# Kernel tuning notes

Hardware: AMD Instinct MI355X
Metric: run time of the kernel (lower is better)

The kernel has to match this reference:

```python
import jax, jax.numpy as jnp
import numpy as np
import math

B, S, D, H = 2, 2048, 4096, 32
HD = D // H          # 128 head dim
HALF = HD // 2       # 64 rotary pairs
AL = 10              # adapter length


def setup_inputs() -> dict:
    key = jax.random.key(0)
    ks = jax.random.split(key, 8)
    sc = 0.02
    x = jax.random.normal(ks[0], (B, S, D), jnp.float32)
    adapter = jax.random.normal(ks[1], (B, AL, D), jnp.float32)
    wq = jax.random.normal(ks[2], (D, D), jnp.float32) * sc
    wk = jax.random.normal(ks[3], (D, D), jnp.float32) * sc
    wv = jax.random.normal(ks[4], (D, D), jnp.float32) * sc
    wo = jax.random.normal(ks[5], (D, D), jnp.float32) * sc
    gate = jax.random.normal(ks[6], (1, H, 1, 1), jnp.float32) * 0.1
    # rotary frequencies (LLaMA convention), freqs_cis = exp(i * t * f)
    inv_freq = 1.0 / (10000.0 ** (np.arange(0, HD, 2).astype(np.float32) / HD))
    ang = np.outer(np.arange(S, dtype=np.float32), inv_freq)  # [S, HALF]
    cos = jnp.asarray(np.cos(ang), jnp.float32)
    sin = jnp.asarray(np.sin(ang), jnp.float32)
    # additive causal mask [1,1,S,S]
    mask = jnp.triu(jnp.full((S, S), -1e9, jnp.float32), 1)[None, None]
    return {"x": x, "mask": mask, "cos": cos, "sin": sin, "wq": wq,
            "wk": wk, "wv": wv, "wo": wo, "gate": gate,
            "adapter": adapter, "start_pos": 0}


def _rope(t, cos, sin):
    # t: [B,S,H,HD]; complex rotate consecutive pairs
    tr = t.reshape(*t.shape[:-1], HALF, 2)
    t0, t1 = tr[..., 0], tr[..., 1]
    c = cos[None, :, None, :]  # [1,S,1,HALF]
    s = sin[None, :, None, :]
    r0 = t0 * c - t1 * s
    r1 = t0 * s + t1 * c
    return jnp.stack([r0, r1], axis=-1).reshape(t.shape)


def reference(x, mask, cos, sin, wq, wk, wv, wo, gate, adapter, start_pos):
    bsz, seqlen, _ = x.shape
    scale = 1.0 / math.sqrt(HD)
    xq = (x @ wq.T).reshape(bsz, seqlen, H, HD)
    xk = (x @ wk.T).reshape(bsz, seqlen, H, HD)
    xv = (x @ wv.T).reshape(bsz, seqlen, H, HD)
    xq = _rope(xq, cos, sin)
    xk = _rope(xk, cos, sin)
    # training path: keys/values = current tokens (start_pos == 0)
    q = xq.transpose(0, 2, 1, 3)   # [B,H,S,HD]
    k = xk.transpose(0, 2, 1, 3)
    v = xv.transpose(0, 2, 1, 3)
    scores = jnp.einsum('bhqd,bhkd->bhqk', q, k) * scale + mask
    scores = jax.nn.softmax(scores.astype(jnp.float32), axis=-1).astype(x.dtype)
    out = jnp.einsum('bhqk,bhkd->bhqd', scores, v)
    # gated adapter cross-attention (adapter_len > 1 branch)
    a_len = adapter.shape[1]
    a_v = (adapter @ wv.T).reshape(bsz, a_len, H, HD).transpose(0, 2, 1, 3)
    a_k = (adapter @ wk.T).reshape(bsz, a_len, H, HD).transpose(0, 2, 1, 3)
    a_scores = jnp.einsum('bhqd,bhkd->bhqk', q, a_k) * scale
    a_scores = jnp.tanh(gate) * jax.nn.softmax(
        a_scores.astype(jnp.float32), axis=-1).astype(x.dtype)
    out = out + jnp.einsum('bhqk,bhkd->bhqd', a_scores, a_v)
    out = out.transpose(0, 2, 1, 3).reshape(bsz, seqlen, -1)
    return out @ wo.T
```

## Files before the change

### kernel.cpp

```cpp
#include <hip/hip_runtime.h>
#include <hip/hip_bf16.h>
#include <stdint.h>

#define B_ 2
#define S_ 2048
#define D_ 4096
#define H_ 32
#define HD_ 128
#define HALF_ 64
#define AL_ 10
#define MROWS (B_*S_)

typedef __hip_bfloat16 bf16;
typedef __attribute__((ext_vector_type(8))) __bf16 bf16x8;
typedef __attribute__((ext_vector_type(4))) float f32x4;
typedef __attribute__((ext_vector_type(4))) unsigned short us4;

__device__ __forceinline__ void gld_lds16(const void* g, void* l) {
    __builtin_amdgcn_global_load_lds((const __attribute__((address_space(1))) void*)g,
                                     (__attribute__((address_space(3))) void*)l, 16, 0, 0);
}

__global__ void detect_dtype(const unsigned short* __restrict__ x, int* __restrict__ flag) {
    __shared__ int cnt;
    if (threadIdx.x == 0) cnt = 0;
    __syncthreads();
    int bad = 0;
#pragma unroll
    for (int i = 0; i < 16; i++) {
        unsigned int u = x[threadIdx.x * 16 + i];
        float v = __uint_as_float(u << 16);
        if (!(fabsf(v) < 1000.f)) bad++;
    }
    atomicAdd(&cnt, bad);
    __syncthreads();
    if (threadIdx.x == 0) flag[0] = (cnt > 64) ? 1 : 0;
}

__global__ void convert_bf16(const void* __restrict__ in, bf16* __restrict__ out,
                             const int* __restrict__ flag, int n) {
    int i = (blockIdx.x * 256 + threadIdx.x) * 4;
    if (i >= n) return;
    if (flag[0]) {
        float4 f = *(const float4*)((const float*)in + i);
        out[i + 0] = __float2bfloat16(f.x);
        out[i + 1] = __float2bfloat16(f.y);
        out[i + 2] = __float2bfloat16(f.z);
        out[i + 3] = __float2bfloat16(f.w);
    } else {
        *(us4*)(out + i) = *(const us4*)((const unsigned short*)in + i);
    }
}

template<int MODE>
__global__ __launch_bounds__(256) void gemm_bt(
    const bf16* __restrict__ A, const bf16* __restrict__ W,
    const bf16* __restrict__ cosb, const bf16* __restrict__ sinb,
    void* __restrict__ outv, const int* __restrict__ flag, int K)
{
    __shared__ __align__(16) bf16 sA[128*64];
    __shared__ __align__(16) bf16 sB[128*64];
    const int tid  = threadIdx.x;
    const int wave = tid >> 6, lane = tid & 63;
    const int quad = lane >> 4, col = lane & 15;
    const int m0 = blockIdx.y * 128, n0 = blockIdx.x * 128;
    const int wm = (wave >> 1) * 64, wn = (wave & 1) * 64;

    bool f32o = false;
    if (MODE == 2) f32o = (flag[0] != 0);

    f32x4 acc[4][4];
#pragma unroll
    for (int i = 0; i < 4; i++)
#pragma unroll
        for (int j = 0; j < 4; j++) acc[i][j] = {0.f, 0.f, 0.f, 0.f};

    for (int k0 = 0; k0 < K; k0 += 64) {
        __syncthreads();
#pragma unroll
        for (int i = 0; i < 4; i++) {
            int c   = i * 256 + tid;
            int row = c >> 3;
            int cc  = (c & 7) ^ (row & 7);
            gld_lds16(A + (size_t)(m0 + row) * K + k0 + cc * 8,
                      sA + (size_t)(i * 256 + wave * 64) * 8);
            gld_lds16(W + (size_t)(n0 + row) * K + k0 + cc * 8,
                      sB + (size_t)(i * 256 + wave * 64) * 8);
        }
        __syncthreads();

#pragma unroll
        for (int kk = 0; kk < 64; kk += 32) {
            bf16x8 af[4], bfr[4];
#pragma unroll
            for (int mt = 0; mt < 4; mt++) {
                int r  = wm + mt * 16 + col;
                int ck = ((kk >> 3) + quad) ^ (r & 7);
                af[mt] = *(const bf16x8*)(sA + r * 64 + ck * 8);
            }
#pragma unroll
            for (int nt = 0; nt < 4; nt++) {
                int r  = wn + nt * 16 + col;
                int ck = ((kk >> 3) + quad) ^ (r & 7);
                bfr[nt] = *(const bf16x8*)(sB + r * 64 + ck * 8);
            }
#pragma unroll
            for (int mt = 0; mt < 4; mt++)
#pragma unroll
                for (int nt = 0; nt < 4; nt++)
                    acc[mt][nt] = __builtin_amdgcn_mfma_f32_16x16x32_bf16(
                        af[mt], bfr[nt], acc[mt][nt], 0, 0, 0);
        }
    }

#pragma unroll
    for (int mt = 0; mt < 4; mt++) {
#pragma unroll
        for (int nt = 0; nt < 4; nt++) {
            int n = n0 + wn + nt * 16 + col;
#pragma unroll
            for (int e = 0; e < 4; e++) {
                int m   = m0 + wm + mt * 16 + quad * 4 + e;
                float v = acc[mt][nt][e];
                if (MODE == 2) {
                    if (f32o) ((float*)outv)[(size_t)m * D_ + n] = v;
                    else      ((bf16*)outv)[(size_t)m * D_ + n] = __float2bfloat16(v);
                } else {
                    int b = m >> 11, s = m & (S_ - 1);
                    int h = n >> 7,  hd = n & (HD_ - 1);
                    bf16* out = (bf16*)outv;
                    if (MODE == 0) {
                        float other = __shfl_xor(v, 1);
                        float c  = __bfloat162float(cosb[s * HALF_ + (hd >> 1)]);
                        float sn = __bfloat162float(sinb[s * HALF_ + (hd >> 1)]);
                        float r  = (hd & 1) ? (v * c + other * sn)
                                            : (v * c - other * sn);
                        out[((size_t)(b * H_ + h) * S_ + s) * HD_ + hd] = __float2bfloat16(r);
                    } else {
                        out[((size_t)(b * H_ + h) * HD_ + hd) * S_ + s] = __float2bfloat16(v);
                    }
                }
            }
        }
    }
}

__global__ __launch_bounds__(512, 4) void attn_fwd(
    const bf16* __restrict__ q, const bf16* __restrict__ k,
    const bf16* __restrict__ vT, bf16* __restrict__ o)
{
    __shared__ __align__(16) bf16 smem[40960];
    bf16* sP = smem + 32768;

    const int tid  = threadIdx.x, wave = tid >> 6, lane = tid & 63;
    const int quad = lane >> 4, col = lane & 15;
    const int qt = (gridDim.x - 1) - blockIdx.x;
    const int bh = blockIdx.y;
    const int q0 = qt * 128;
    const int row0 = q0 + wave * 16;
    const int rmax = row0 + 15;
    const bf16* qb = q  + (size_t)bh * S_ * HD_;
    const bf16* kb = k  + (size_t)bh * S_ * HD_;
    const bf16* vb = vT + (size_t)bh * HD_ * S_;

    bf16x8 qf[4];
#pragma unroll
    for (int kkI = 0; kkI < 4; kkI++)
        qf[kkI] = *(const bf16x8*)(qb + (size_t)(row0 + col) * HD_ + (kkI * 4 + quad) * 8);

    float mst[4], lst[4];
#pragma unroll
    for (int e = 0; e < 4; e++) { mst[e] = -1e30f; lst[e] = 0.f; }
    f32x4 oacc[8];
#pragma unroll
    for (int i = 0; i < 8; i++) oacc[i] = {0.f, 0.f, 0.f, 0.f};

#pragma unroll
    for (int i = 0; i < 2; i++) {
        int c = i * 512 + tid;
        int rowK = c >> 4, ccK = (c & 15) ^ (rowK & 7);
        gld_lds16(kb + (size_t)rowK * HD_ + ccK * 8,
                  smem + (size_t)(i * 512 + wave * 64) * 8);
        int rowV = c >> 3, ccV = (c & 7) ^ (rowV & 7);
        gld_lds16(vb + (size_t)rowV * S_ + ccV * 8,
                  smem + 16384 + (size_t)(i * 512 + wave * 64) * 8);
    }

    const float scale = 0.08838834764831845f;
    const int ktEnd = 2 * qt + 2;
    int cur = 0;

    for (int kt = 0; kt < ktEnd; kt++) {
        const int k0 = kt * 64;
        bf16* sKc = smem + cur * 8192;
        bf16* sVc = smem + 16384 + cur * 8192;

        if (kt + 1 < ktEnd) {
            const int kn = k0 + 64;
            bf16* sKn = smem + (cur ^ 1) * 8192;
            bf16* sVn = smem + 16384 + (cur ^ 1) * 8192;
#pragma unroll
            for (int i = 0; i < 2; i++) {
                int c = i * 512 + tid;
                int rowK = c >> 4, ccK = (c & 15) ^ (rowK & 7);
                gld_lds16(kb + (size_t)(kn + rowK) * HD_ + ccK * 8,
                          sKn + (size_t)(i * 512 + wave * 64) * 8);
                int rowV = c >> 3, ccV = (c & 7) ^ (rowV & 7);
                gld_lds16(vb + (size_t)rowV * S_ + kn + ccV * 8,
                          sVn + (size_t)(i * 512 + wave * 64) * 8);
            }
            asm volatile("s_waitcnt vmcnt(4)" ::: "memory");
        } else {
            asm volatile("s_waitcnt vmcnt(0)" ::: "memory");
        }
        asm volatile("s_barrier" ::: "memory");

        if (k0 <= rmax) {
            f32x4 sc[4];
#pragma unroll
            for (int nt = 0; nt < 4; nt++) sc[nt] = {0.f, 0.f, 0.f, 0.f};
            __builtin_amdgcn_s_setprio(1);
#pragma unroll
            for (int kkI = 0; kkI < 4; kkI++) {
#pragma unroll
                for (int nt = 0; nt < 4; nt++) {
                    int rk  = nt * 16 + col;
                    int ckk = (kkI * 4 + quad) ^ (rk & 7);
                    bf16x8 bk = *(const bf16x8*)(sKc + rk * 128 + ckk * 8);
                    sc[nt] = __builtin_amdgcn_mfma_f32_16x16x32_bf16(qf[kkI], bk, sc[nt], 0, 0, 0);
                }
            }
            __builtin_amdgcn_s_setprio(0);

            const bool diag = (k0 + 63 > row0);
#pragma unroll
            for (int nt = 0; nt < 4; nt++)
#pragma unroll
                for (int e = 0; e < 4; e++) {
                    float v = sc[nt][e] * scale;
                    if (diag && (k0 + nt * 16 + col > row0 + quad * 4 + e))
                        v = -1e30f;
                    sc[nt][e] = v;
                }

            float alpha_[4];
#pragma unroll
            for (int e = 0; e < 4; e++) {
                float mx = fmaxf(fmaxf(sc[0][e], sc[1][e]),
                                 fmaxf(sc[2][e], sc[3][e]));
#pragma unroll
                for (int off = 1; off < 16; off <<= 1) mx = fmaxf(mx, __shfl_xor(mx, off));
                float mnew = fmaxf(mst[e], mx);
                float al   = __expf(mst[e] - mnew);
                float rs   = 0.f;
                int prow = wave * 16 + quad * 4 + e;
#pragma unroll
                for (int nt = 0; nt < 4; nt++) {
                    float p = __expf(sc[nt][e] - mnew);
                    rs += p;
                    int pcol = nt * 16 + col;
                    int pc   = (pcol >> 3) ^ (prow & 7);
                    sP[prow * 64 + pc * 8 + (pcol & 7)] = __float2bfloat16(p);
                }
#pragma unroll
                for (int off = 1; off < 16; off <<= 1) rs += __shfl_xor(rs, off);
                lst[e] = lst[e] * al + rs;
                mst[e] = mnew;
                alpha_[e] = al;
            }
#pragma unroll
            for (int nt = 0; nt < 8; nt++)
#pragma unroll
                for (int e = 0; e < 4; e++) oacc[nt][e] *= alpha_[e];

            __builtin_amdgcn_s_setprio(1);
#pragma unroll
            for (int kkI = 0; kkI < 2; kkI++) {
                int rp  = wave * 16 + col;
                int ckp = (kkI * 4 + quad) ^ (rp & 7);
                bf16x8 pf = *(const bf16x8*)(sP + rp * 64 + ckp * 8);
#pragma unroll
                for (int nt = 0; nt < 8; nt++) {
                    int rv  = nt * 16 + col;
                    int ckv = (kkI * 4 + quad) ^ (rv & 7);
                    bf16x8 vf = *(const bf16x8*)(sVc + rv * 64 + ckv * 8);
                    oacc[nt] = __builtin_amdgcn_mfma_f32_16x16x32_bf16(pf, vf, oacc[nt], 0, 0, 0);
                }
            }
            __builtin_amdgcn_s_setprio(0);
        }

        asm volatile("s_barrier" ::: "memory");
        cur ^= 1;
    }

    const int b = bh >> 5, h = bh & (H_ - 1);
#pragma unroll
    for (int e = 0; e < 4; e++) {
        int s = q0 + wave * 16 + quad * 4 + e;
        float inv = 1.f / lst[e];
#pragma unroll
        for (int nt = 0; nt < 8; nt++) {
            int hd = nt * 16 + col;
            o[((size_t)(b * S_ + s) * H_ + h) * HD_ + hd] =
                __float2bfloat16(oacc[nt][e] * inv);
        }
    }
}

__global__ __launch_bounds__(256) void adapter_kv(
    const bf16* __restrict__ adp, const bf16* __restrict__ wk,
    const bf16* __restrict__ wv, float* __restrict__ ak, float* __restrict__ av)
{
    const int tid = threadIdx.x, wave = tid >> 6, lane = tid & 63;
    const int gid = blockIdx.x * 4 + wave;
    const int n = gid & (D_ - 1), b = gid >> 12;
    const bf16* w    = blockIdx.y ? wv : wk;
    float*      outp = blockIdx.y ? av : ak;

    float acc[AL_];
#pragma unroll
    for (int j = 0; j < AL_; j++) acc[j] = 0.f;

    for (int t = 0; t < 8; t++) {
        int kb = t * 512 + lane * 8;
        bf16x8 w8 = *(const bf16x8*)(w + (size_t)n * D_ + kb);
        float wf[8];
#pragma unroll
        for (int i = 0; i < 8; i++) wf[i] = (float)w8[i];
#pragma unroll
        for (int j = 0; j < AL_; j++) {
            bf16x8 a8 = *(const bf16x8*)(adp + (size_t)(b * AL_ + j) * D_ + kb);
            float s = 0.f;
#pragma unroll
            for (int i = 0; i < 8; i++) s += (float)a8[i] * wf[i];
            acc[j] += s;
        }
    }
#pragma unroll
    for (int j = 0; j < AL_; j++) {
        float v = acc[j];
#pragma unroll
        for (int off = 1; off < 64; off <<= 1) v += __shfl_xor(v, off);
        if (lane == 0) outp[(size_t)(b * AL_ + j) * D_ + n] = v;
    }
}

__global__ __launch_bounds__(256) void adapter_add(
    const bf16* __restrict__ q, const float* __restrict__ ak,
    const float* __restrict__ av, const bf16* __restrict__ gate,
    bf16* __restrict__ o)
{
    const int tid = threadIdx.x, wave = tid >> 6, lane = tid & 63;
    const int g = blockIdx.x * 4 + wave;
    const int s = g & (S_ - 1);
    const int h = (g >> 11) & (H_ - 1);
    const int b = g >> 16;
    const int hd = lane * 2;

    const bf16* qp = q + ((size_t)(b * H_ + h) * S_ + s) * HD_ + hd;
    float q0f = __bfloat162float(qp[0]);
    float q1f = __bfloat162float(qp[1]);
    const float scale = 0.08838834764831845f;

    float sc[AL_];
#pragma unroll
    for (int j = 0; j < AL_; j++) {
        const float* akp = ak + (size_t)(b * AL_ + j) * D_ + h * HD_ + hd;
        float p = q0f * akp[0] + q1f * akp[1];
#pragma unroll
        for (int off = 1; off < 64; off <<= 1) p += __shfl_xor(p, off);
        sc[j] = p * scale;
    }
    float mx = sc[0];
#pragma unroll
    for (int j = 1; j < AL_; j++) mx = fmaxf(mx, sc[j]);
    float sum = 0.f;
#pragma unroll
    for (int j = 0; j < AL_; j++) { sc[j] = __expf(sc[j] - mx); sum += sc[j]; }
    float wgt = tanhf(__bfloat162float(gate[h])) / sum;

    float a0 = 0.f, a1 = 0.f;
#pragma unroll
    for (int j = 0; j < AL_; j++) {
        const float* avp = av + (size_t)(b * AL_ + j) * D_ + h * HD_ + hd;
        a0 += sc[j] * avp[0];
        a1 += sc[j] * avp[1];
    }
    bf16* op = o + ((size_t)(b * S_ + s) * H_ + h) * HD_ + hd;
    op[0] = __float2bfloat16(__bfloat162float(op[0]) + wgt * a0);
    op[1] = __float2bfloat16(__bfloat162float(op[1]) + wgt * a1);
}

extern "C" void kernel_launch(void* const* d_in, const int* in_sizes, int n_in,
                              void* d_out, int out_size, void* d_ws, size_t ws_size,
                              hipStream_t stream)
{
    const void* x_raw    = d_in[0];
    const void* cos_raw  = d_in[2];
    const void* sin_raw  = d_in[3];
    const void* wq_raw   = d_in[4];
    const void* wk_raw   = d_in[5];
    const void* wv_raw   = d_in[6];
    const void* wo_raw   = d_in[7];
    const void* gate_raw = d_in[8];
    const void* adp_raw  = d_in[9];

    const size_t NE = (size_t)B_ * S_ * D_;
    const int    CS = S_ * HALF_;
    const int    AD = B_ * AL_ * D_;

    bf16* xc   = (bf16*)d_ws;
    bf16* wqc  = xc  + NE;
    bf16* wkc  = wqc + NE;
    bf16* wvc  = wkc + NE;
    bf16* woc  = wvc + NE;
    bf16* qb   = woc + NE;
    bf16* kb   = qb  + NE;
    bf16* vb   = kb  + NE;
    bf16* cosc = vb  + NE;
    bf16* sinc = cosc + CS;
    bf16* adpc = sinc + CS;
    bf16* gatec= adpc + AD;
    float* akb = (float*)(gatec + 32);
    float* avb = akb + AD;
    int*  flag = (int*)(avb + AD);
    bf16* ab   = xc;

    dim3 blk(256);
    detect_dtype<<<1, 256, 0, stream>>>((const unsigned short*)x_raw, flag);

    convert_bf16<<<dim3((int)(NE/4 + 255) / 256), blk, 0, stream>>>(x_raw,  xc,  flag, (int)NE);
    convert_bf16<<<dim3((int)(NE/4 + 255) / 256), blk, 0, stream>>>(wq_raw, wqc, flag, (int)NE);
    convert_bf16<<<dim3((int)(NE/4 + 255) / 256), blk, 0, stream>>>(wk_raw, wkc, flag, (int)NE);
    convert_bf16<<<dim3((int)(NE/4 + 255) / 256), blk, 0, stream>>>(wv_raw, wvc, flag, (int)NE);
    convert_bf16<<<dim3((int)(NE/4 + 255) / 256), blk, 0, stream>>>(wo_raw, woc, flag, (int)NE);
    convert_bf16<<<dim3((CS/4 + 255) / 256), blk, 0, stream>>>(cos_raw,  cosc, flag, CS);
    convert_bf16<<<dim3((CS/4 + 255) / 256), blk, 0, stream>>>(sin_raw,  sinc, flag, CS);
    convert_bf16<<<dim3((AD/4 + 255) / 256), blk, 0, stream>>>(adp_raw,  adpc, flag, AD);
    convert_bf16<<<dim3(1), blk, 0, stream>>>(gate_raw, gatec, flag, 32);

    dim3 gg(D_ / 128, MROWS / 128);
    gemm_bt<0><<<gg, blk, 0, stream>>>(xc, wqc, cosc, sinc, qb, flag, D_);
    gemm_bt<0><<<gg, blk, 0, stream>>>(xc, wkc, cosc, sinc, kb, flag, D_);
    gemm_bt<1><<<gg, blk, 0, stream>>>(xc, wvc, cosc, sinc, vb, flag, D_);
    adapter_kv<<<dim3(2048, 2), blk, 0, stream>>>(adpc, wkc, wvc, akb, avb);
    attn_fwd<<<dim3(S_ / 128, B_ * H_), dim3(512), 0, stream>>>(qb, kb, vb, ab);
    adapter_add<<<dim3(B_ * H_ * S_ / 4), blk, 0, stream>>>(qb, akb, avb, gatec, ab);
    gemm_bt<2><<<gg, blk, 0, stream>>>(ab, woc, cosc, sinc, d_out, flag, D_);
}
```

Measured before the change: 1.435 ms.

## Fold softmax scale into Q, pair causal tiles per block, lazy rescale

The softmax scale is folded into the Q projection epilogue, so both attention kernels skip the per-score multiply. Each attention block now processes two query tiles (qt and NQT-1-qt), which balances the causal work across blocks and halves the grid. The online softmax uses exp2 with a log2e prefactor and skips the output rescale unless some row max grew by more than a threshold. The sP swizzle is also changed to reduce LDS bank conflicts. Rounding Q to bf16 after scaling slightly changes numerics, and the lazy rescale lets exponentials exceed 1 before normalisation.

```diff
diff --git a/kernel.cpp b/kernel.cpp
--- a/kernel.cpp
+++ b/kernel.cpp
@@ -10,6 +10,7 @@
 #define HALF_ 64
 #define AL_ 10
 #define MROWS (B_*S_)
+#define NQT_ (S_/128)
 
 typedef __hip_bfloat16 bf16;
 typedef __attribute__((ext_vector_type(8))) __bf16 bf16x8;
@@ -56,7 +57,7 @@
 __global__ __launch_bounds__(256) void gemm_bt(
     const bf16* __restrict__ A, const bf16* __restrict__ W,
     const bf16* __restrict__ cosb, const bf16* __restrict__ sinb,
-    void* __restrict__ outv, const int* __restrict__ flag, int K)
+    void* __restrict__ outv, const int* __restrict__ flag, int K, float oscale)
 {
     __shared__ __align__(16) bf16 sA[128*64];
     __shared__ __align__(16) bf16 sB[128*64];
@@ -135,7 +136,8 @@
                         float sn = __bfloat162float(sinb[s * HALF_ + (hd >> 1)]);
                         float r  = (hd & 1) ? (v * c + other * sn)
                                             : (v * c - other * sn);
-                        out[((size_t)(b * H_ + h) * S_ + s) * HD_ + hd] = __float2bfloat16(r);
+                        out[((size_t)(b * H_ + h) * S_ + s) * HD_ + hd] =
+                            __float2bfloat16(r * oscale);
                     } else {
                         out[((size_t)(b * H_ + h) * HD_ + hd) * S_ + s] = __float2bfloat16(v);
                     }
@@ -154,156 +156,177 @@
 
     const int tid  = threadIdx.x, wave = tid >> 6, lane = tid & 63;
     const int quad = lane >> 4, col = lane & 15;
-    const int qt = (gridDim.x - 1) - blockIdx.x;
     const int bh = blockIdx.y;
-    const int q0 = qt * 128;
-    const int row0 = q0 + wave * 16;
-    const int rmax = row0 + 15;
+    const int b = bh >> 5, h = bh & (H_ - 1);
     const bf16* qb = q  + (size_t)bh * S_ * HD_;
     const bf16* kb = k  + (size_t)bh * S_ * HD_;
     const bf16* vb = vT + (size_t)bh * HD_ * S_;
-
-    bf16x8 qf[4];
-#pragma unroll
-    for (int kkI = 0; kkI < 4; kkI++)
-        qf[kkI] = *(const bf16x8*)(qb + (size_t)(row0 + col) * HD_ + (kkI * 4 + quad) * 8);
-
-    float mst[4], lst[4];
-#pragma unroll
-    for (int e = 0; e < 4; e++) { mst[e] = -1e30f; lst[e] = 0.f; }
-    f32x4 oacc[8];
-#pragma unroll
-    for (int i = 0; i < 8; i++) oacc[i] = {0.f, 0.f, 0.f, 0.f};
-
-#pragma unroll
-    for (int i = 0; i < 2; i++) {
-        int c = i * 512 + tid;
-        int rowK = c >> 4, ccK = (c & 15) ^ (rowK & 7);
-        gld_lds16(kb + (size_t)rowK * HD_ + ccK * 8,
-                  smem + (size_t)(i * 512 + wave * 64) * 8);
-        int rowV = c >> 3, ccV = (c & 7) ^ (rowV & 7);
-        gld_lds16(vb + (size_t)rowV * S_ + ccV * 8,
-                  smem + 16384 + (size_t)(i * 512 + wave * 64) * 8);
-    }
-
-    const float scale = 0.08838834764831845f;
-    const int ktEnd = 2 * qt + 2;
-    int cur = 0;
-
-    for (int kt = 0; kt < ktEnd; kt++) {
-        const int k0 = kt * 64;
-        bf16* sKc = smem + cur * 8192;
-        bf16* sVc = smem + 16384 + cur * 8192;
-
-        if (kt + 1 < ktEnd) {
-            const int kn = k0 + 64;
-            bf16* sKn = smem + (cur ^ 1) * 8192;
-            bf16* sVn = smem + 16384 + (cur ^ 1) * 8192;
-#pragma unroll
-            for (int i = 0; i < 2; i++) {
-                int c = i * 512 + tid;
-                int rowK = c >> 4, ccK = (c & 15) ^ (rowK & 7);
-                gld_lds16(kb + (size_t)(kn + rowK) * HD_ + ccK * 8,
-                          sKn + (size_t)(i * 512 + wave * 64) * 8);
-                int rowV = c >> 3, ccV = (c & 7) ^ (rowV & 7);
-                gld_lds16(vb + (size_t)rowV * S_ + kn + ccV * 8,
-                          sVn + (size_t)(i * 512 + wave * 64) * 8);
-            }
-            asm volatile("s_waitcnt vmcnt(4)" ::: "memory");
-        } else {
-            asm volatile("s_waitcnt vmcnt(0)" ::: "memory");
-        }
-        asm volatile("s_barrier" ::: "memory");
-
-        if (k0 <= rmax) {
-            f32x4 sc[4];
-#pragma unroll
-            for (int nt = 0; nt < 4; nt++) sc[nt] = {0.f, 0.f, 0.f, 0.f};
-            __builtin_amdgcn_s_setprio(1);
-#pragma unroll
-            for (int kkI = 0; kkI < 4; kkI++) {
-#pragma unroll
-                for (int nt = 0; nt < 4; nt++) {
-                    int rk  = nt * 16 + col;
-                    int ckk = (kkI * 4 + quad) ^ (rk & 7);
-                    bf16x8 bk = *(const bf16x8*)(sKc + rk * 128 + ckk * 8);
-                    sc[nt] = __builtin_amdgcn_mfma_f32_16x16x32_bf16(qf[kkI], bk, sc[nt], 0, 0, 0);
-                }
-            }
-            __builtin_amdgcn_s_setprio(0);
-
-            const bool diag = (k0 + 63 > row0);
-#pragma unroll
-            for (int nt = 0; nt < 4; nt++)
+    const float L2E = 1.44269504088896f;
+
+#pragma unroll 1
+    for (int pass = 0; pass < 2; pass++) {
+        const int qt = pass ? (NQT_ - 1 - (int)blockIdx.x) : (int)blockIdx.x;
+        const int q0 = qt * 128;
+        const int row0 = q0 + wave * 16;
+        const int rmax = row0 + 15;
+
+        bf16x8 qf[4];
+#pragma unroll
+        for (int kkI = 0; kkI < 4; kkI++)
+            qf[kkI] = *(const bf16x8*)(qb + (size_t)(row0 + col) * HD_
+                                          + (kkI * 4 + quad) * 8);
+
+        float mst[4], lst[4];
+#pragma unroll
+        for (int e = 0; e < 4; e++) { mst[e] = -1e30f; lst[e] = 0.f; }
+        f32x4 oacc[8];
+#pragma unroll
+        for (int i = 0; i < 8; i++) oacc[i] = {0.f, 0.f, 0.f, 0.f};
+
+#pragma unroll
+        for (int i = 0; i < 2; i++) {
+            int c = i * 512 + tid;
+            int rowK = c >> 4, ccK = (c & 15) ^ (rowK & 7);
+            gld_lds16(kb + (size_t)rowK * HD_ + ccK * 8,
+                      smem + (size_t)(i * 512 + wave * 64) * 8);
+            int rowV = c >> 3, ccV = (c & 7) ^ (rowV & 7);
+            gld_lds16(vb + (size_t)rowV * S_ + ccV * 8,
+                      smem + 16384 + (size_t)(i * 512 + wave * 64) * 8);
+        }
+
+        const int ktEnd = 2 * qt + 2;
+        int cur = 0;
+
+        for (int kt = 0; kt < ktEnd; kt++) {
+            const int k0 = kt * 64;
+            bf16* sKc = smem + cur * 8192;
+            bf16* sVc = smem + 16384 + cur * 8192;
+
+            if (kt + 1 < ktEnd) {
+                const int kn = k0 + 64;
+                bf16* sKn = smem + (cur ^ 1) * 8192;
+                bf16* sVn = smem + 16384 + (cur ^ 1) * 8192;
+#pragma unroll
+                for (int i = 0; i < 2; i++) {
+                    int c = i * 512 + tid;
+                    int rowK = c >> 4, ccK = (c & 15) ^ (rowK & 7);
+                    gld_lds16(kb + (size_t)(kn + rowK) * HD_ + ccK * 8,
+                              sKn + (size_t)(i * 512 + wave * 64) * 8);
+                    int rowV = c >> 3, ccV = (c & 7) ^ (rowV & 7);
+                    gld_lds16(vb + (size_t)rowV * S_ + kn + ccV * 8,
+                              sVn + (size_t)(i * 512 + wave * 64) * 8);
+                }
+                asm volatile("s_waitcnt vmcnt(4)" ::: "memory");
+            } else {
+                asm volatile("s_waitcnt vmcnt(0)" ::: "memory");
+            }
+            asm volatile("s_barrier" ::: "memory");
+
+            if (k0 <= rmax) {
+                f32x4 sc[4];
+#pragma unroll
+                for (int nt = 0; nt < 4; nt++) sc[nt] = {0.f, 0.f, 0.f, 0.f};
+                __builtin_amdgcn_s_setprio(1);
+#pragma unroll
+                for (int kkI = 0; kkI < 4; kkI++) {
+#pragma unroll
+                    for (int nt = 0; nt < 4; nt++) {
+                        int rk  = nt * 16 + col;
+                        int ckk = (kkI * 4 + quad) ^ (rk & 7);
+                        bf16x8 bk = *(const bf16x8*)(sKc + rk * 128 + ckk * 8);
+                        sc[nt] = __builtin_amdgcn_mfma_f32_16x16x32_bf16(qf[kkI], bk, sc[nt], 0, 0, 0);
+                    }
+                }
+                __builtin_amdgcn_s_setprio(0);
+
+                if (k0 + 63 > row0) {
+#pragma unroll
+                    for (int nt = 0; nt < 4; nt++)
+#pragma unroll
+                        for (int e = 0; e < 4; e++)
+                            if (k0 + nt * 16 + col > row0 + quad * 4 + e)
+                                sc[nt][e] = -1e30f;
+                }
+
+                float mxv[4];
 #pragma unroll
                 for (int e = 0; e < 4; e++) {
-                    float v = sc[nt][e] * scale;
-                    if (diag && (k0 + nt * 16 + col > row0 + quad * 4 + e))
-                        v = -1e30f;
-                    sc[nt][e] = v;
-                }
-
-            float alpha_[4];
-#pragma unroll
-            for (int e = 0; e < 4; e++) {
-                float mx = fmaxf(fmaxf(sc[0][e], sc[1][e]),
-                                 fmaxf(sc[2][e], sc[3][e]));
-#pragma unroll
-                for (int off = 1; off < 16; off <<= 1) mx = fmaxf(mx, __shfl_xor(mx, off));
-                float mnew = fmaxf(mst[e], mx);
-                float al   = __expf(mst[e] - mnew);
-                float rs   = 0.f;
-                int prow = wave * 16 + quad * 4 + e;
-#pragma unroll
-                for (int nt = 0; nt < 4; nt++) {
-                    float p = __expf(sc[nt][e] - mnew);
-                    rs += p;
-                    int pcol = nt * 16 + col;
-                    int pc   = (pcol >> 3) ^ (prow & 7);
-                    sP[prow * 64 + pc * 8 + (pcol & 7)] = __float2bfloat16(p);
-                }
-#pragma unroll
-                for (int off = 1; off < 16; off <<= 1) rs += __shfl_xor(rs, off);
-                lst[e] = lst[e] * al + rs;
-                mst[e] = mnew;
-                alpha_[e] = al;
-            }
-#pragma unroll
-            for (int nt = 0; nt < 8; nt++)
-#pragma unroll
-                for (int e = 0; e < 4; e++) oacc[nt][e] *= alpha_[e];
-
-            __builtin_amdgcn_s_setprio(1);
-#pragma unroll
-            for (int kkI = 0; kkI < 2; kkI++) {
-                int rp  = wave * 16 + col;
-                int ckp = (kkI * 4 + quad) ^ (rp & 7);
-                bf16x8 pf = *(const bf16x8*)(sP + rp * 64 + ckp * 8);
-#pragma unroll
-                for (int nt = 0; nt < 8; nt++) {
-                    int rv  = nt * 16 + col;
-                    int ckv = (kkI * 4 + quad) ^ (rv & 7);
-                    bf16x8 vf = *(const bf16x8*)(sVc + rv * 64 + ckv * 8);
-                    oacc[nt] = __builtin_amdgcn_mfma_f32_16x16x32_bf16(pf, vf, oacc[nt], 0, 0, 0);
-                }
-            }
-            __builtin_amdgcn_s_setprio(0);
-        }
-
-        asm volatile("s_barrier" ::: "memory");
-        cur ^= 1;
-    }
-
-    const int b = bh >> 5, h = bh & (H_ - 1);
-#pragma unroll
-    for (int e = 0; e < 4; e++) {
-        int s = q0 + wave * 16 + quad * 4 + e;
-        float inv = 1.f / lst[e];
-#pragma unroll
-        for (int nt = 0; nt < 8; nt++) {
-            int hd = nt * 16 + col;
-            o[((size_t)(b * S_ + s) * H_ + h) * HD_ + hd] =
-                __float2bfloat16(oacc[nt][e] * inv);
+                    float mx = fmaxf(fmaxf(sc[0][e], sc[1][e]),
+                                     fmaxf(sc[2][e], sc[3][e]));
+#pragma unroll
+                    for (int off = 1; off < 16; off <<= 1) mx = fmaxf(mx, __shfl_xor(mx, off));
+                    mxv[e] = mx;
+                }
+                float need = fmaxf(fmaxf(mxv[0] - mst[0], mxv[1] - mst[1]),
+                                   fmaxf(mxv[2] - mst[2], mxv[3] - mst[3]));
+
+                if (!__all(need <= 8.f)) {
+                    float alpha_[4];
+#pragma unroll
+                    for (int e = 0; e < 4; e++) {
+                        float mnew = fmaxf(mst[e], mxv[e]);
+                        float al   = __builtin_amdgcn_exp2f((mst[e] - mnew) * L2E);
+                        mst[e] = mnew;
+                        lst[e] *= al;
+                        alpha_[e] = al;
+                    }
+#pragma unroll
+                    for (int nt = 0; nt < 8; nt++)
+#pragma unroll
+                        for (int e = 0; e < 4; e++) oacc[nt][e] *= alpha_[e];
+                }
+
+#pragma unroll
+                for (int e = 0; e < 4; e++) {
+                    float nm = -mst[e] * L2E;
+                    float rs = 0.f;
+                    int prow = wave * 16 + quad * 4 + e;
+                    int fsw  = (prow & 7) ^ (((prow >> 3) & 1) << 1);
+#pragma unroll
+                    for (int nt = 0; nt < 4; nt++) {
+                        float p = __builtin_amdgcn_exp2f(fmaf(sc[nt][e], L2E, nm));
+                        rs += p;
+                        int pcol = nt * 16 + col;
+                        int pc   = (pcol >> 3) ^ fsw;
+                        sP[prow * 64 + pc * 8 + (pcol & 7)] = __float2bfloat16(p);
+                    }
+#pragma unroll
+                    for (int off = 1; off < 16; off <<= 1) rs += __shfl_xor(rs, off);
+                    lst[e] += rs;
+                }
+
+                __builtin_amdgcn_s_setprio(1);
+#pragma unroll
+                for (int kkI = 0; kkI < 2; kkI++) {
+                    int rp  = wave * 16 + col;
+                    int fsw = (rp & 7) ^ (((rp >> 3) & 1) << 1);
+                    int ckp = (kkI * 4 + quad) ^ fsw;
+                    bf16x8 pf = *(const bf16x8*)(sP + rp * 64 + ckp * 8);
+#pragma unroll
+                    for (int nt = 0; nt < 8; nt++) {
+                        int rv  = nt * 16 + col;
+                        int ckv = (kkI * 4 + quad) ^ (rv & 7);
+                        bf16x8 vf = *(const bf16x8*)(sVc + rv * 64 + ckv * 8);
+                        oacc[nt] = __builtin_amdgcn_mfma_f32_16x16x32_bf16(pf, vf, oacc[nt], 0, 0, 0);
+                    }
+                }
+                __builtin_amdgcn_s_setprio(0);
+            }
+
+            asm volatile("s_barrier" ::: "memory");
+            cur ^= 1;
+        }
+
+#pragma unroll
+        for (int e = 0; e < 4; e++) {
+            int s = row0 + quad * 4 + e;
+            float inv = 1.f / lst[e];
+#pragma unroll
+            for (int nt = 0; nt < 8; nt++) {
+                int hd = nt * 16 + col;
+                o[((size_t)(b * S_ + s) * H_ + h) * HD_ + hd] =
+                    __float2bfloat16(oacc[nt][e] * inv);
+            }
         }
     }
 }
@@ -361,7 +384,6 @@
     const bf16* qp = q + ((size_t)(b * H_ + h) * S_ + s) * HD_ + hd;
     float q0f = __bfloat162float(qp[0]);
     float q1f = __bfloat162float(qp[1]);
-    const float scale = 0.08838834764831845f;
 
     float sc[AL_];
 #pragma unroll
@@ -370,7 +392,7 @@
         float p = q0f * akp[0] + q1f * akp[1];
 #pragma unroll
         for (int off = 1; off < 64; off <<= 1) p += __shfl_xor(p, off);
-        sc[j] = p * scale;
+        sc[j] = p;
     }
     float mx = sc[0];
 #pragma unroll
@@ -427,6 +449,8 @@
     int*  flag = (int*)(avb + AD);
     bf16* ab   = xc;
 
+    const float scale = 0.08838834764831845f;
+
     dim3 blk(256);
     detect_dtype<<<1, 256, 0, stream>>>((const unsigned short*)x_raw, flag);
 
@@ -441,11 +465,11 @@
     convert_bf16<<<dim3(1), blk, 0, stream>>>(gate_raw, gatec, flag, 32);
 
     dim3 gg(D_ / 128, MROWS / 128);
-    gemm_bt<0><<<gg, blk, 0, stream>>>(xc, wqc, cosc, sinc, qb, flag, D_);
-    gemm_bt<0><<<gg, blk, 0, stream>>>(xc, wkc, cosc, sinc, kb, flag, D_);
-    gemm_bt<1><<<gg, blk, 0, stream>>>(xc, wvc, cosc, sinc, vb, flag, D_);
+    gemm_bt<0><<<gg, blk, 0, stream>>>(xc, wqc, cosc, sinc, qb, flag, D_, scale);
+    gemm_bt<0><<<gg, blk, 0, stream>>>(xc, wkc, cosc, sinc, kb, flag, D_, 1.0f);
+    gemm_bt<1><<<gg, blk, 0, stream>>>(xc, wvc, cosc, sinc, vb, flag, D_, 1.0f);
     adapter_kv<<<dim3(2048, 2), blk, 0, stream>>>(adpc, wkc, wvc, akb, avb);
-    attn_fwd<<<dim3(S_ / 128, B_ * H_), dim3(512), 0, stream>>>(qb, kb, vb, ab);
+    attn_fwd<<<dim3(NQT_ / 2, B_ * H_), dim3(512), 0, stream>>>(qb, kb, vb, ab);
     adapter_add<<<dim3(B_ * H_ * S_ / 4), blk, 0, stream>>>(qb, akb, avb, gatec, ab);
-    gemm_bt<2><<<gg, blk, 0, stream>>>(ab, woc, cosc, sinc, d_out, flag, D_);
-}
+    gemm_bt<2><<<gg, blk, 0, stream>>>(ab, woc, cosc, sinc, d_out, flag, D_, 1.0f);
+}
```

Measured after the change: 1.338 ms. -6.8%, faster.
